# Performance work log

Hardware: AMD Instinct MI355X
Metric: run time of the kernel (lower is better)

## Reference

```python
import jax, jax.numpy as jnp
import numpy as np

B, T, C, H = 2, 2048, 1024, 16
D = C // H
EPS = 1e-5

def _layer_norm(x, w, b):
    mu = jnp.mean(x, axis=-1, keepdims=True)
    var = jnp.var(x, axis=-1, keepdims=True)
    return (x - mu) * jax.lax.rsqrt(var + EPS) * w + b

def setup_inputs() -> dict:
    key = jax.random.key(0)
    ks = jax.random.split(key, 8)
    s = 0.02
    return {
        "x": jax.random.normal(ks[0], (B, T, C), jnp.float32),
        "ln1_w": jnp.ones((C,), jnp.float32),
        "ln1_b": jnp.zeros((C,), jnp.float32),
        "wq": jax.random.normal(ks[1], (C, C), jnp.float32) * s,
        "bq": jnp.zeros((C,), jnp.float32),
        "wk": jax.random.normal(ks[2], (C, C), jnp.float32) * s,
        "bk": jnp.zeros((C,), jnp.float32),
        "wv": jax.random.normal(ks[3], (C, C), jnp.float32) * s,
        "bv": jnp.zeros((C,), jnp.float32),
        "wo": jax.random.normal(ks[4], (C, C), jnp.float32) * s,
        "bo": jnp.zeros((C,), jnp.float32),
        "ln2_w": jnp.ones((C,), jnp.float32),
        "ln2_b": jnp.zeros((C,), jnp.float32),
        "w1": jax.random.normal(ks[5], (C, 4 * C), jnp.float32) * s,
        "b1": jnp.zeros((4 * C,), jnp.float32),
        "w2": jax.random.normal(ks[6], (4 * C, C), jnp.float32) * s,
        "b2": jnp.zeros((C,), jnp.float32),
    }

def reference(x, ln1_w, ln1_b, wq, bq, wk, bk, wv, bv, wo, bo,
              ln2_w, ln2_b, w1, b1, w2, b2):
    # --- attention branch ---
    h = _layer_norm(x, ln1_w, ln1_b)
    q = (h @ wq + bq).reshape(B, T, H, D).transpose(0, 2, 1, 3)  # [B,H,T,D]
    k = (h @ wk + bk).reshape(B, T, H, D).transpose(0, 2, 1, 3)
    v = (h @ wv + bv).reshape(B, T, H, D).transpose(0, 2, 1, 3)
    att = jnp.einsum("bhqd,bhkd->bhqk", q, k) * (1.0 / np.sqrt(D))
    causal = jnp.tril(jnp.ones((T, T), dtype=bool))
    att = jnp.where(causal[None, None], att, jnp.float32(-jnp.inf))
    att = jax.nn.softmax(att, axis=-1)
    y = jnp.einsum("bhqk,bhkd->bhqd", att, v)
    y = y.transpose(0, 2, 1, 3).reshape(B, T, C)
    y = y @ wo + bo
    x = x + y
    # --- MLP branch ---
    h = _layer_norm(x, ln2_w, ln2_b)
    h = jax.nn.gelu(h @ w1 + b1, approximate=False)
    h = h @ w2 + b2
    return x + h
```

## Files before the change

### kernel.cpp

```cpp
#include <hip/hip_runtime.h>
#include <hip/hip_bf16.h>
#include <math.h>

#define B_  2
#define T_  2048
#define C_  1024
#define H_  16
#define D_  64
#define BT_ (B_*T_)

typedef __hip_bfloat16 bf16;
typedef short bf16x8 __attribute__((ext_vector_type(8)));
typedef float floatx4 __attribute__((ext_vector_type(4)));

struct alignas(8) bf4 { bf16 v[4]; };

#define GLOAD_LDS16(g, l) __builtin_amdgcn_global_load_lds(            \
    (const __attribute__((address_space(1))) void*)(g),                \
    (__attribute__((address_space(3))) void*)(l), 16, 0, 0)

__global__ __launch_bounds__(256) void ln_bf16_kernel(const float* __restrict__ x,
    const float* __restrict__ w, const float* __restrict__ b,
    bf16* __restrict__ out)
{
    __shared__ float ps[4], ps2[4];
    __shared__ float sm, srs;
    const int row = blockIdx.x;
    const int tid = threadIdx.x;
    float4 v = ((const float4*)(x + (size_t)row * C_))[tid];
    float s  = v.x + v.y + v.z + v.w;
    float s2 = v.x*v.x + v.y*v.y + v.z*v.z + v.w*v.w;
    for (int off = 32; off > 0; off >>= 1) {
        s  += __shfl_down(s,  off);
        s2 += __shfl_down(s2, off);
    }
    const int wid = tid >> 6;
    if ((tid & 63) == 0) { ps[wid] = s; ps2[wid] = s2; }
    __syncthreads();
    if (tid == 0) {
        float ts  = ps[0] + ps[1] + ps[2] + ps[3];
        float ts2 = ps2[0] + ps2[1] + ps2[2] + ps2[3];
        float mean = ts * (1.0f / C_);
        float var  = ts2 * (1.0f / C_) - mean * mean;
        sm  = mean;
        srs = rsqrtf(var + 1e-5f);
    }
    __syncthreads();
    const float mean = sm, rs = srs;
    float4 wv = ((const float4*)w)[tid];
    float4 bv = ((const float4*)b)[tid];
    bf4 o;
    o.v[0] = __float2bfloat16((v.x - mean) * rs * wv.x + bv.x);
    o.v[1] = __float2bfloat16((v.y - mean) * rs * wv.y + bv.y);
    o.v[2] = __float2bfloat16((v.z - mean) * rs * wv.z + bv.z);
    o.v[3] = __float2bfloat16((v.w - mean) * rs * wv.w + bv.w);
    *(bf4*)(out + (size_t)row * C_ + tid * 4) = o;
}

__device__ __forceinline__ void wconv_body(const float* __restrict__ W,
    bf16* __restrict__ Wt, int K, int N, int k0, int n0)
{
    __shared__ float L[64][65];
    const int t = threadIdx.x;
    const int r = t >> 4, c4 = t & 15;
    #pragma unroll
    for (int p = 0; p < 4; ++p) {
        const int kr = p * 16 + r;
        const float4 v = *(const float4*)(W + (size_t)(k0 + kr) * N + n0 + c4 * 4);
        L[kr][c4*4+0] = v.x; L[kr][c4*4+1] = v.y;
        L[kr][c4*4+2] = v.z; L[kr][c4*4+3] = v.w;
    }
    __syncthreads();
    #pragma unroll
    for (int p = 0; p < 4; ++p) {
        const int nr = p * 16 + r;
        bf4 o;
        o.v[0] = __float2bfloat16(L[c4*4+0][nr]);
        o.v[1] = __float2bfloat16(L[c4*4+1][nr]);
        o.v[2] = __float2bfloat16(L[c4*4+2][nr]);
        o.v[3] = __float2bfloat16(L[c4*4+3][nr]);
        *(bf4*)(Wt + (size_t)(n0 + nr) * K + k0 + c4 * 4) = o;
    }
}

__global__ __launch_bounds__(256) void wconv_t_kernel(const float* __restrict__ W,
    bf16* __restrict__ Wt, int K, int N)
{
    wconv_body(W, Wt, K, N, blockIdx.x * 64, blockIdx.y * 64);
}

__global__ __launch_bounds__(256) void wconv4_kernel(
    const float* __restrict__ wq, const float* __restrict__ wk,
    const float* __restrict__ wv, const float* __restrict__ wo,
    bf16* __restrict__ wqkvT, bf16* __restrict__ woT)
{
    const int z = blockIdx.z;
    const float* W = (z == 0) ? wq : (z == 1) ? wk : (z == 2) ? wv : wo;
    bf16* Wt = (z == 3) ? woT : wqkvT + (size_t)z * 1024 * 1024;
    wconv_body(W, Wt, 1024, 1024, blockIdx.x * 64, blockIdx.y * 64);
}

__global__ void bcat_kernel(const float* __restrict__ bq, const float* __restrict__ bk,
                            const float* __restrict__ bv, float* __restrict__ o)
{
    const int i = blockIdx.x * 256 + threadIdx.x;
    float v = (i < 1024) ? bq[i] : (i < 2048 ? bk[i - 1024] : bv[i - 2048]);
    o[i] = v;
}

__global__ __launch_bounds__(256) void splitk_reduce_kernel(
    float* __restrict__ out, const float* __restrict__ p1,
    const float* __restrict__ bias, const float* __restrict__ res)
{
    const size_t i = (size_t)blockIdx.x * 256 + threadIdx.x;
    float4 o = ((const float4*)out)[i];
    const float4 p = ((const float4*)p1)[i];
    const float4 bb = ((const float4*)bias)[i & (C_ / 4 - 1)];
    const float4 xx = ((const float4*)res)[i];
    o.x += p.x + bb.x + xx.x;
    o.y += p.y + bb.y + xx.y;
    o.z += p.z + bb.z + xx.z;
    o.w += p.w + bb.w + xx.w;
    ((float4*)out)[i] = o;
}

template<int TM, int TN>
__global__ __launch_bounds__(256) void mfma_gemm_t(
    const bf16* __restrict__ A, const bf16* __restrict__ Wt,
    const float* __restrict__ bias, const float* __restrict__ res,
    void* __restrict__ outv, bf16* __restrict__ vT, float* __restrict__ psplit,
    int M, int N, int K, int ldk, int mode)
{
    constexpr int MI = TM / 32;
    constexpr int NJ = TN / 32;
    constexpr int NSLOT = (TM + TN) / 64;
    __shared__ __align__(16) bf16 As[TM * 32];
    __shared__ __align__(16) bf16 Bs[TN * 32];
    const int tid = threadIdx.x;
    const int w = tid >> 6, l = tid & 63;
    const int fm = l & 15, qd = l >> 4;
    const int m0 = blockIdx.x * TM, n0 = blockIdx.y * TN;
    const int bz = blockIdx.z;
    const int wr = (w >> 1) * (TM / 2), wc = (w & 1) * (TN / 2);

    const bf16* Ab = A  + (size_t)bz * K;
    const bf16* Wb = Wt + (size_t)bz * K;

    const bf16* gsrc[NSLOT];
    bf16* ldst[NSLOT];
    #pragma unroll
    for (int p = 0; p < NSLOT; ++p) {
        const int s = tid + p * 256;
        if (s < TM * 4) {
            const int row = s >> 2, ch = (s & 3) ^ ((row >> 1) & 3);
            gsrc[p] = Ab + (size_t)(m0 + row) * ldk + ch * 8;
            ldst[p] = As + s * 8;
        } else {
            const int s2 = s - TM * 4;
            const int row = s2 >> 2, ch = (s2 & 3) ^ ((row >> 1) & 3);
            gsrc[p] = Wb + (size_t)(n0 + row) * ldk + ch * 8;
            ldst[p] = Bs + s2 * 8;
        }
    }

    floatx4 acc[MI][NJ] = {};
    const int sw = (qd ^ ((fm >> 1) & 3)) * 8;

    const int nk = K >> 5;
    for (int kk = 0; kk < nk; ++kk) {
        const size_t ko = (size_t)kk * 32;
        __syncthreads();
        #pragma unroll
        for (int p = 0; p < NSLOT; ++p)
            GLOAD_LDS16(gsrc[p] + ko, ldst[p]);
        __syncthreads();
        bf16x8 af[MI], bfr[NJ];
        #pragma unroll
        for (int i = 0; i < MI; ++i)
            af[i] = *(const bf16x8*)(As + (wr + i * 16 + fm) * 32 + sw);
        #pragma unroll
        for (int j = 0; j < NJ; ++j)
            bfr[j] = *(const bf16x8*)(Bs + (wc + j * 16 + fm) * 32 + sw);
        #pragma unroll
        for (int i = 0; i < MI; ++i)
            #pragma unroll
            for (int j = 0; j < NJ; ++j)
                acc[i][j] = __builtin_amdgcn_mfma_f32_16x16x32_bf16(
                    af[i], bfr[j], acc[i][j], 0, 0, 0);
    }

    const int col0 = n0 + wc;
    const int row0 = m0 + wr;
    const bool isv = (mode == 3) && (col0 >= 2048);
    float* po = (mode == 4) ? (bz ? psplit : (float*)outv) : nullptr;
    #pragma unroll
    for (int j = 0; j < NJ; ++j) {
        const int col = col0 + j * 16 + fm;
        const float bb = bias[col];
        const bool isq = (mode == 3) && (col0 + j * 16 < 1024);
        #pragma unroll
        for (int i = 0; i < MI; ++i) {
            const int row = row0 + i * 16 + qd * 4;
            floatx4 a = acc[i][j];
            if (mode == 4) {
                #pragma unroll
                for (int r = 0; r < 4; ++r)
                    po[(size_t)(row + r) * N + col] = a[r];
            } else if (mode == 2) {
                float* o = (float*)outv;
                #pragma unroll
                for (int r = 0; r < 4; ++r)
                    o[(size_t)(row + r) * N + col] =
                        a[r] + bb + res[(size_t)(row + r) * N + col];
            } else if (isv) {
                bf4 pv;
                #pragma unroll
                for (int r = 0; r < 4; ++r) pv.v[r] = __float2bfloat16(a[r] + bb);
                *(bf4*)(vT + (size_t)(col - 2048) * M + row) = pv;
            } else {
                bf16* o = (bf16*)outv;
                #pragma unroll
                for (int r = 0; r < 4; ++r) {
                    float vv = a[r] + bb;
                    if (mode == 1) vv = 0.5f * vv * (1.0f + erff(vv * 0.70710678118f));
                    if (isq) vv *= 0.125f;
                    o[(size_t)(row + r) * N + col] = __float2bfloat16(vv);
                }
            }
        }
    }
}

__global__ __launch_bounds__(256) void attn_mfma_kernel(
    const bf16* __restrict__ qkv, const bf16* __restrict__ vT,
    bf16* __restrict__ y)
{
    const int pi = blockIdx.x, h = blockIdx.y, b = blockIdx.z;
    const int tid = threadIdx.x, w = tid >> 6, l = tid & 63;
    const int fm = l & 15, qd = l >> 4;
    const int qta = pi, qtb = 31 - pi;
    const float M0 = 3.0f;

    __shared__ __align__(16) bf16 Ks[4096];
    __shared__ __align__(16) bf16 Vs[4096];
    __shared__ __align__(16) bf16 Ps[8][1152];

    const int r0 = tid >> 2,         c0 = (tid & 3) ^ ((r0 >> 1) & 3);
    const int r1 = (tid + 256) >> 2, c1 = ((tid + 256) & 3) ^ ((r1 >> 1) & 3);
    const bf16* kbase = qkv + (size_t)(b * T_) * 3072 + 1024 + h * 64;
    const bf16* vbase = vT + (size_t)(h * 64) * BT_ + b * T_;
    const bf16* kg0 = kbase + (size_t)(r0 & 63) * 3072 + (r0 >> 6) * 32 + c0 * 8;
    const bf16* kg1 = kbase + (size_t)(r1 & 63) * 3072 + (r1 >> 6) * 32 + c1 * 8;
    const bf16* vg0 = vbase + (size_t)(r0 & 63) * BT_ + (r0 >> 6) * 32 + c0 * 8;
    const bf16* vg1 = vbase + (size_t)(r1 & 63) * BT_ + (r1 >> 6) * 32 + c1 * 8;
    bf16* ksl0 = Ks + (size_t)(w * 64) * 8;
    bf16* ksl1 = Ks + (size_t)(w * 64 + 256) * 8;
    bf16* vsl0 = Vs + (size_t)(w * 64) * 8;
    bf16* vsl1 = Vs + (size_t)(w * 64 + 256) * 8;

    const bf16* qpa = qkv + (size_t)(b * T_ + qta * 64 + w * 16 + fm) * 3072 + h * 64 + qd * 8;
    const bf16* qpb = qkv + (size_t)(b * T_ + qtb * 64 + w * 16 + fm) * 3072 + h * 64 + qd * 8;
    const bf16x8 qa0 = *(const bf16x8*)qpa, qa1 = *(const bf16x8*)(qpa + 32);
    const bf16x8 qb0 = *(const bf16x8*)qpb, qb1 = *(const bf16x8*)(qpb + 32);

    const int qba = qta * 64 + w * 16 + qd * 4;
    const int qbb = qtb * 64 + w * 16 + qd * 4;
    const int sw = (qd ^ ((fm >> 1) & 3)) * 8;

    float la[4] = {}, lb[4] = {};
    floatx4 Oa[4] = {}, Ob[4] = {};
    bf16* psa = &Ps[w * 2][0];
    bf16* psb = &Ps[w * 2 + 1][0];

    auto tile = [&](const bf16x8 q0, const bf16x8 q1, float* lsum,
                    floatx4* O, bf16* ps, const int kt, const int qt, const int qb) {
        floatx4 S[4];
        #pragma unroll
        for (int nt = 0; nt < 4; ++nt) {
            const int rr = nt * 16 + fm;
            const bf16x8 k0 = *(const bf16x8*)(Ks + rr * 32 + sw);
            const bf16x8 k1 = *(const bf16x8*)(Ks + (64 + rr) * 32 + sw);
            floatx4 s = {};
            s = __builtin_amdgcn_mfma_f32_16x16x32_bf16(q0, k0, s, 0, 0, 0);
            s = __builtin_amdgcn_mfma_f32_16x16x32_bf16(q1, k1, s, 0, 0, 0);
            S[nt] = s;
        }
        if (kt == qt) {
            #pragma unroll
            for (int nt = 0; nt < 4; ++nt) {
                const int key = kt * 64 + nt * 16 + fm;
                #pragma unroll
                for (int r = 0; r < 4; ++r)
                    if (key > qb + r) S[nt][r] = -1e30f;
            }
        }
        #pragma unroll
        for (int nt = 0; nt < 4; ++nt)
            #pragma unroll
            for (int r = 0; r < 4; ++r) {
                const float p = __expf(S[nt][r] - M0);
                lsum[r] += p;
                ps[(qd * 4 + r) * 72 + nt * 16 + fm] = __float2bfloat16(p);
            }
        #pragma unroll
        for (int s2 = 0; s2 < 2; ++s2) {
            const bf16x8 pf = *(const bf16x8*)(ps + fm * 72 + s2 * 32 + qd * 8);
            #pragma unroll
            for (int nt = 0; nt < 4; ++nt) {
                const bf16x8 vf =
                    *(const bf16x8*)(Vs + (s2 * 64 + nt * 16 + fm) * 32 + sw);
                O[nt] = __builtin_amdgcn_mfma_f32_16x16x32_bf16(pf, vf, O[nt], 0, 0, 0);
            }
        }
    };

    for (int kt = 0; kt <= qtb; ++kt) {
        const size_t kOff = (size_t)kt * 64 * 3072;
        const size_t vOff = (size_t)kt * 64;
        __syncthreads();
        GLOAD_LDS16(kg0 + kOff, ksl0);
        GLOAD_LDS16(kg1 + kOff, ksl1);
        GLOAD_LDS16(vg0 + vOff, vsl0);
        GLOAD_LDS16(vg1 + vOff, vsl1);
        __syncthreads();
        tile(qb0, qb1, lb, Ob, psb, kt, qtb, qbb);
        if (kt <= qta)
            tile(qa0, qa1, la, Oa, psa, kt, qta, qba);
    }

    #pragma unroll
    for (int mk = 1; mk < 16; mk <<= 1)
        #pragma unroll
        for (int r = 0; r < 4; ++r) {
            la[r] += __shfl_xor(la[r], mk);
            lb[r] += __shfl_xor(lb[r], mk);
        }

    #pragma unroll
    for (int r = 0; r < 4; ++r) {
        const float inva = 1.0f / la[r];
        const float invb = 1.0f / lb[r];
        const size_t rowa = (size_t)(b * T_) + qba + r;
        const size_t rowb = (size_t)(b * T_) + qbb + r;
        #pragma unroll
        for (int nt = 0; nt < 4; ++nt) {
            y[rowa * C_ + h * 64 + nt * 16 + fm] = __float2bfloat16(Oa[nt][r] * inva);
            y[rowb * C_ + h * 64 + nt * 16 + fm] = __float2bfloat16(Ob[nt][r] * invb);
        }
    }
}

extern "C" void kernel_launch(void* const* d_in, const int* in_sizes, int n_in,
                              void* d_out, int out_size, void* d_ws, size_t ws_size,
                              hipStream_t stream)
{
    const float* x     = (const float*)d_in[0];
    const float* ln1_w = (const float*)d_in[1];
    const float* ln1_b = (const float*)d_in[2];
    const float* wq    = (const float*)d_in[3];
    const float* bq    = (const float*)d_in[4];
    const float* wk    = (const float*)d_in[5];
    const float* bk    = (const float*)d_in[6];
    const float* wv    = (const float*)d_in[7];
    const float* bv    = (const float*)d_in[8];
    const float* wo    = (const float*)d_in[9];
    const float* bo    = (const float*)d_in[10];
    const float* ln2_w = (const float*)d_in[11];
    const float* ln2_b = (const float*)d_in[12];
    const float* w1    = (const float*)d_in[13];
    const float* b1    = (const float*)d_in[14];
    const float* w2    = (const float*)d_in[15];
    const float* b2    = (const float*)d_in[16];
    float* out = (float*)d_out;

    char* ws = (char*)d_ws;
    const size_t MB = 1024 * 1024;
    bf16*  wqkvT = (bf16*)(ws);
    bf16*  woT   = (bf16*)(ws + 6 * MB);
    bf16*  w1T   = (bf16*)(ws + 8 * MB);
    bf16*  w2T   = (bf16*)(ws + 16 * MB);
    float* bqkv  = (float*)(ws + 24 * MB);
    bf16*  h     = (bf16*)(ws + 24 * MB + 65536);
    bf16*  qkv   = (bf16*)(ws + 32 * MB + 65536);
    bf16*  vT    = (bf16*)(ws + 56 * MB + 65536);
    bf16*  y     = (bf16*)(ws + 64 * MB + 65536);
    float* x2    = (float*)(ws + 72 * MB + 65536);
    bf16*  u     = qkv;
    float* p1    = (float*)ws;

    wconv4_kernel<<<dim3(16, 16, 4), 256, 0, stream>>>(wq, wk, wv, wo, wqkvT, woT);
    wconv_t_kernel<<<dim3(16, 64), 256, 0, stream>>>(w1, w1T, 1024, 4096);
    wconv_t_kernel<<<dim3(64, 16), 256, 0, stream>>>(w2, w2T, 4096, 1024);
    bcat_kernel<<<12, 256, 0, stream>>>(bq, bk, bv, bqkv);

    ln_bf16_kernel<<<BT_, 256, 0, stream>>>(x, ln1_w, ln1_b, h);
    mfma_gemm_t<128, 128><<<dim3(32, 24), 256, 0, stream>>>(
        h, wqkvT, bqkv, nullptr, qkv, vT, nullptr, BT_, 3072, C_, C_, 3);
    attn_mfma_kernel<<<dim3(16, H_, B_), 256, 0, stream>>>(qkv, vT, y);
    mfma_gemm_t<128, 64><<<dim3(32, 16), 256, 0, stream>>>(
        y, woT, bo, x, x2, nullptr, nullptr, BT_, C_, C_, C_, 2);

    ln_bf16_kernel<<<BT_, 256, 0, stream>>>(x2, ln2_w, ln2_b, h);
    mfma_gemm_t<128, 128><<<dim3(32, 32), 256, 0, stream>>>(
        h, w1T, b1, nullptr, u, nullptr, nullptr, BT_, 4 * C_, C_, C_, 1);
    mfma_gemm_t<128, 128><<<dim3(32, 8, 2), 256, 0, stream>>>(
        u, w2T, b2, nullptr, out, nullptr, p1, BT_, C_, 2 * C_, 4 * C_, 4);
    splitk_reduce_kernel<<<BT_ * C_ / 1024, 256, 0, stream>>>(out, p1, b2, x2);
}
```

Measured before the change: 398.5 us.

## Deepen GEMM K-tile to 64, fuse w1/w2 conversions, use tanh GELU

```diff
diff --git a/kernel.cpp b/kernel.cpp
--- a/kernel.cpp
+++ b/kernel.cpp
@@ -83,12 +83,6 @@
     }
 }
 
-__global__ __launch_bounds__(256) void wconv_t_kernel(const float* __restrict__ W,
-    bf16* __restrict__ Wt, int K, int N)
-{
-    wconv_body(W, Wt, K, N, blockIdx.x * 64, blockIdx.y * 64);
-}
-
 __global__ __launch_bounds__(256) void wconv4_kernel(
     const float* __restrict__ wq, const float* __restrict__ wk,
     const float* __restrict__ wv, const float* __restrict__ wo,
@@ -98,6 +92,16 @@
     const float* W = (z == 0) ? wq : (z == 1) ? wk : (z == 2) ? wv : wo;
     bf16* Wt = (z == 3) ? woT : wqkvT + (size_t)z * 1024 * 1024;
     wconv_body(W, Wt, 1024, 1024, blockIdx.x * 64, blockIdx.y * 64);
+}
+
+__global__ __launch_bounds__(256) void wconv2_kernel(
+    const float* __restrict__ w1, const float* __restrict__ w2,
+    bf16* __restrict__ w1T, bf16* __restrict__ w2T)
+{
+    if (blockIdx.z == 0)
+        wconv_body(w1, w1T, 1024, 4096, blockIdx.x * 64, blockIdx.y * 64);
+    else
+        wconv_body(w2, w2T, 4096, 1024, blockIdx.y * 64, blockIdx.x * 64);
 }
 
 __global__ void bcat_kernel(const float* __restrict__ bq, const float* __restrict__ bk,
@@ -124,7 +128,7 @@
     ((float4*)out)[i] = o;
 }
 
-template<int TM, int TN>
+template<int TM, int TN, int BK>
 __global__ __launch_bounds__(256) void mfma_gemm_t(
     const bf16* __restrict__ A, const bf16* __restrict__ Wt,
     const float* __restrict__ bias, const float* __restrict__ res,
@@ -133,9 +137,10 @@
 {
     constexpr int MI = TM / 32;
     constexpr int NJ = TN / 32;
-    constexpr int NSLOT = (TM + TN) / 64;
-    __shared__ __align__(16) bf16 As[TM * 32];
-    __shared__ __align__(16) bf16 Bs[TN * 32];
+    constexpr int CPR = BK / 8;
+    constexpr int NSLOT = (TM + TN) * CPR / 256;
+    __shared__ __align__(16) bf16 As[TM * BK];
+    __shared__ __align__(16) bf16 Bs[TN * BK];
     const int tid = threadIdx.x;
     const int w = tid >> 6, l = tid & 63;
     const int fm = l & 15, qd = l >> 4;
@@ -151,48 +156,57 @@
     #pragma unroll
     for (int p = 0; p < NSLOT; ++p) {
         const int s = tid + p * 256;
-        if (s < TM * 4) {
-            const int row = s >> 2, ch = (s & 3) ^ ((row >> 1) & 3);
+        if (s < TM * CPR) {
+            const int row = s / CPR, pos = s % CPR;
+            const int ch = pos ^ (row & (CPR - 1));
             gsrc[p] = Ab + (size_t)(m0 + row) * ldk + ch * 8;
             ldst[p] = As + s * 8;
         } else {
-            const int s2 = s - TM * 4;
-            const int row = s2 >> 2, ch = (s2 & 3) ^ ((row >> 1) & 3);
+            const int s2 = s - TM * CPR;
+            const int row = s2 / CPR, pos = s2 % CPR;
+            const int ch = pos ^ (row & (CPR - 1));
             gsrc[p] = Wb + (size_t)(n0 + row) * ldk + ch * 8;
             ldst[p] = Bs + s2 * 8;
         }
     }
 
     floatx4 acc[MI][NJ] = {};
-    const int sw = (qd ^ ((fm >> 1) & 3)) * 8;
-
-    const int nk = K >> 5;
+
+    const int nk = K / BK;
     for (int kk = 0; kk < nk; ++kk) {
-        const size_t ko = (size_t)kk * 32;
+        const size_t ko = (size_t)kk * BK;
         __syncthreads();
         #pragma unroll
         for (int p = 0; p < NSLOT; ++p)
             GLOAD_LDS16(gsrc[p] + ko, ldst[p]);
         __syncthreads();
-        bf16x8 af[MI], bfr[NJ];
-        #pragma unroll
-        for (int i = 0; i < MI; ++i)
-            af[i] = *(const bf16x8*)(As + (wr + i * 16 + fm) * 32 + sw);
-        #pragma unroll
-        for (int j = 0; j < NJ; ++j)
-            bfr[j] = *(const bf16x8*)(Bs + (wc + j * 16 + fm) * 32 + sw);
-        #pragma unroll
-        for (int i = 0; i < MI; ++i)
-            #pragma unroll
-            for (int j = 0; j < NJ; ++j)
-                acc[i][j] = __builtin_amdgcn_mfma_f32_16x16x32_bf16(
-                    af[i], bfr[j], acc[i][j], 0, 0, 0);
+        #pragma unroll
+        for (int ks = 0; ks < BK / 32; ++ks) {
+            bf16x8 af[MI], bfr[NJ];
+            #pragma unroll
+            for (int i = 0; i < MI; ++i) {
+                const int row = wr + i * 16 + fm;
+                af[i] = *(const bf16x8*)(As + row * BK
+                        + (((ks * 4 + qd) ^ (row & (CPR - 1))) * 8));
+            }
+            #pragma unroll
+            for (int j = 0; j < NJ; ++j) {
+                const int row = wc + j * 16 + fm;
+                bfr[j] = *(const bf16x8*)(Bs + row * BK
+                        + (((ks * 4 + qd) ^ (row & (CPR - 1))) * 8));
+            }
+            #pragma unroll
+            for (int i = 0; i < MI; ++i)
+                #pragma unroll
+                for (int j = 0; j < NJ; ++j)
+                    acc[i][j] = __builtin_amdgcn_mfma_f32_16x16x32_bf16(
+                        af[i], bfr[j], acc[i][j], 0, 0, 0);
+        }
     }
 
     const int col0 = n0 + wc;
     const int row0 = m0 + wr;
     const bool isv = (mode == 3) && (col0 >= 2048);
-    float* po = (mode == 4) ? (bz ? psplit : (float*)outv) : nullptr;
     #pragma unroll
     for (int j = 0; j < NJ; ++j) {
         const int col = col0 + j * 16 + fm;
@@ -203,9 +217,10 @@
             const int row = row0 + i * 16 + qd * 4;
             floatx4 a = acc[i][j];
             if (mode == 4) {
+                float* o = bz ? psplit : (float*)outv;
                 #pragma unroll
                 for (int r = 0; r < 4; ++r)
-                    po[(size_t)(row + r) * N + col] = a[r];
+                    o[(size_t)(row + r) * N + col] = a[r];
             } else if (mode == 2) {
                 float* o = (float*)outv;
                 #pragma unroll
@@ -222,7 +237,12 @@
                 #pragma unroll
                 for (int r = 0; r < 4; ++r) {
                     float vv = a[r] + bb;
-                    if (mode == 1) vv = 0.5f * vv * (1.0f + erff(vv * 0.70710678118f));
+                    if (mode == 1) {
+                        float zz = vv * (0.7978845608f + 0.0356774081f * vv * vv);
+                        zz = fminf(zz, 15.0f);
+                        const float e = __expf(2.0f * zz);
+                        vv = vv * (e / (e + 1.0f));
+                    }
                     if (isq) vv *= 0.125f;
                     o[(size_t)(row + r) * N + col] = __float2bfloat16(vv);
                 }
@@ -389,21 +409,20 @@
     float* p1    = (float*)ws;
 
     wconv4_kernel<<<dim3(16, 16, 4), 256, 0, stream>>>(wq, wk, wv, wo, wqkvT, woT);
-    wconv_t_kernel<<<dim3(16, 64), 256, 0, stream>>>(w1, w1T, 1024, 4096);
-    wconv_t_kernel<<<dim3(64, 16), 256, 0, stream>>>(w2, w2T, 4096, 1024);
+    wconv2_kernel<<<dim3(16, 64, 2), 256, 0, stream>>>(w1, w2, w1T, w2T);
     bcat_kernel<<<12, 256, 0, stream>>>(bq, bk, bv, bqkv);
 
     ln_bf16_kernel<<<BT_, 256, 0, stream>>>(x, ln1_w, ln1_b, h);
-    mfma_gemm_t<128, 128><<<dim3(32, 24), 256, 0, stream>>>(
+    mfma_gemm_t<128, 128, 64><<<dim3(32, 24), 256, 0, stream>>>(
         h, wqkvT, bqkv, nullptr, qkv, vT, nullptr, BT_, 3072, C_, C_, 3);
     attn_mfma_kernel<<<dim3(16, H_, B_), 256, 0, stream>>>(qkv, vT, y);
-    mfma_gemm_t<128, 64><<<dim3(32, 16), 256, 0, stream>>>(
+    mfma_gemm_t<128, 64, 64><<<dim3(32, 16), 256, 0, stream>>>(
         y, woT, bo, x, x2, nullptr, nullptr, BT_, C_, C_, C_, 2);
 
     ln_bf16_kernel<<<BT_, 256, 0, stream>>>(x2, ln2_w, ln2_b, h);
-    mfma_gemm_t<128, 128><<<dim3(32, 32), 256, 0, stream>>>(
+    mfma_gemm_t<128, 128, 64><<<dim3(32, 32), 256, 0, stream>>>(
         h, w1T, b1, nullptr, u, nullptr, nullptr, BT_, 4 * C_, C_, C_, 1);
-    mfma_gemm_t<128, 128><<<dim3(32, 8, 2), 256, 0, stream>>>(
+    mfma_gemm_t<128, 128, 64><<<dim3(32, 8, 2), 256, 0, stream>>>(
         u, w2T, b2, nullptr, out, nullptr, p1, BT_, C_, 2 * C_, 4 * C_, 4);
     splitk_reduce_kernel<<<BT_ * C_ / 1024, 256, 0, stream>>>(out, p1, b2, x2);
 }
```

After: 365.8 us. -8.2%, faster.
